# Performance work log

Measured on AMD Instinct MI355X. Metric: run time of the kernel, lower is better.

The kernel has to match this reference:

```python
import jax, jax.numpy as jnp
import numpy as np

INPUT_DIM = 1024
EMBED_DIM = 1024
NUM_HEADS = 16
HEAD_DIM = EMBED_DIM // NUM_HEADS


def setup_inputs() -> dict:
    key = jax.random.key(0)
    k_x, k_qkv, k_w, k_b = jax.random.split(key, 4)
    B, N = 2, 2048
    x = jax.random.normal(k_x, (B, N, INPUT_DIM), dtype=jnp.float32)
    # nn.Linear weights: stored [out, in]; scale like torch default init
    s1 = 1.0 / np.sqrt(INPUT_DIM)
    s2 = 1.0 / np.sqrt(EMBED_DIM)
    W_qkv = jax.random.uniform(k_qkv, (3 * EMBED_DIM, INPUT_DIM), jnp.float32, -s1, s1)
    W_out = jax.random.uniform(k_w, (EMBED_DIM, EMBED_DIM), jnp.float32, -s2, s2)
    b_out = jax.random.uniform(k_b, (EMBED_DIM,), jnp.float32, -s2, s2)
    return {"x": x, "W_qkv": W_qkv, "W_out": W_out, "b_out": b_out}


def reference(x, W_qkv, W_out, b_out):
    B, N, C = x.shape
    # qkv projection (no bias): [B, N, 3*embed]
    qkv = jnp.einsum('bnc,ec->bne', x, W_qkv)
    q = qkv[:, :, 0:EMBED_DIM].reshape(B, N, NUM_HEADS, HEAD_DIM)
    k = qkv[:, :, EMBED_DIM:2 * EMBED_DIM].reshape(B, N, NUM_HEADS, HEAD_DIM)
    v = qkv[:, :, 2 * EMBED_DIM:3 * EMBED_DIM].reshape(B, N, NUM_HEADS, HEAD_DIM)
    scores = jnp.einsum('bihd,bjhd->bhij', q, k) / jnp.sqrt(jnp.float32(HEAD_DIM))
    attn = jax.nn.softmax(scores, axis=-1)
    out = jnp.einsum('bhij,bjhd->bihd', attn, v).reshape(B, N, EMBED_DIM)
    return jnp.einsum('bne,oe->bno', out, W_out) + b_out
```

## Files before the change

kernel.cpp:

```cpp
#include <hip/hip_runtime.h>
#include <stdint.h>

typedef __attribute__((ext_vector_type(8))) short short8;
typedef __attribute__((ext_vector_type(4))) short bf16x4;
typedef __attribute__((ext_vector_type(4))) float f32x4;

#define MFMA32(a, b, c) __builtin_amdgcn_mfma_f32_16x16x32_bf16((a), (b), (c), 0, 0, 0)

__device__ __forceinline__ uint16_t f32_to_bf16(float f) {
  union { float f; uint32_t u; } v; v.f = f;
  uint32_t u = v.u;
  u += 0x7FFFu + ((u >> 16) & 1u);
  return (uint16_t)(u >> 16);
}
__device__ __forceinline__ uint16_t f32_to_bf16_fast(float f) {
  union { float f; uint32_t u; } v; v.f = f;
  return (uint16_t)((v.u + 0x8000u) >> 16);
}

__device__ __forceinline__ void load_lds16(const uint16_t* g, uint16_t* l) {
  __builtin_amdgcn_global_load_lds(
      (const __attribute__((address_space(1))) uint32_t*)g,
      (__attribute__((address_space(3))) uint32_t*)l, 16, 0, 0);
}

__global__ __launch_bounds__(256) void cvt3_kernel(
    const float* __restrict__ x, const float* __restrict__ w1,
    const float* __restrict__ w2, uint16_t* __restrict__ xb,
    uint16_t* __restrict__ w1b, uint16_t* __restrict__ w2b) {
  const int i = blockIdx.x * 256 + threadIdx.x;
  const float4* src;
  ushort4* dst;
  int off;
  if (i < 1048576) { src = (const float4*)x;  dst = (ushort4*)xb;  off = i; }
  else if (i < 1835008) { src = (const float4*)w1; dst = (ushort4*)w1b; off = i - 1048576; }
  else { src = (const float4*)w2; dst = (ushort4*)w2b; off = i - 1835008; }
  const float4 v = src[off];
  ushort4 o;
  o.x = f32_to_bf16(v.x);
  o.y = f32_to_bf16(v.y);
  o.z = f32_to_bf16(v.z);
  o.w = f32_to_bf16(v.w);
  dst[off] = o;
}

__global__ __launch_bounds__(256) void gemm_qkv_kernel(
    const uint16_t* __restrict__ A, const uint16_t* __restrict__ Bt,
    uint16_t* __restrict__ Qh, uint16_t* __restrict__ Kh, uint16_t* __restrict__ Vh) {
  __shared__ __align__(16) uint16_t As[128 * 64];
  __shared__ __align__(16) uint16_t Bs[128 * 64];
  const int tid = threadIdx.x;
  const int wave = tid >> 6;
  const int lane = tid & 63;
  const int quad = lane >> 4;
  const int l16 = lane & 15;
  const int row0 = blockIdx.x * 128;
  const int col0 = blockIdx.y * 128;
  const int wm = (wave >> 1) * 64;
  const int wn = (wave & 1) * 64;
  const int K = 1024;

  f32x4 acc[4][4];
#pragma unroll
  for (int a = 0; a < 4; ++a)
#pragma unroll
    for (int b = 0; b < 4; ++b) acc[a][b] = (f32x4){0.f, 0.f, 0.f, 0.f};

  const int swz8 = ((lane & 7) ^ ((lane >> 3) & 7)) * 8;
  const uint16_t* gA = A + (size_t)(row0 + wave * 32 + (lane >> 3)) * K + swz8;
  const uint16_t* gB = Bt + (size_t)(col0 + wave * 32 + (lane >> 3)) * K + swz8;

  for (int k0 = 0; k0 < K; k0 += 64) {
#pragma unroll
    for (int s = 0; s < 4; ++s) {
      load_lds16(gA + (size_t)s * 8 * K + k0, &As[(wave * 32 + s * 8) * 64]);
      load_lds16(gB + (size_t)s * 8 * K + k0, &Bs[(wave * 32 + s * 8) * 64]);
    }
    __syncthreads();
#pragma unroll
    for (int ks = 0; ks < 2; ++ks) {
      const int cswz = (((ks * 4 + quad) ^ (l16 & 7)) * 8);
      short8 af[4], bf[4];
#pragma unroll
      for (int mt = 0; mt < 4; ++mt)
        af[mt] = *(const short8*)&As[(wm + mt * 16 + l16) * 64 + cswz];
#pragma unroll
      for (int nt = 0; nt < 4; ++nt)
        bf[nt] = *(const short8*)&Bs[(wn + nt * 16 + l16) * 64 + cswz];
#pragma unroll
      for (int mt = 0; mt < 4; ++mt)
#pragma unroll
        for (int nt = 0; nt < 4; ++nt)
          acc[mt][nt] = MFMA32(af[mt], bf[nt], acc[mt][nt]);
    }
    __syncthreads();
  }

#pragma unroll
  for (int mt = 0; mt < 4; ++mt) {
#pragma unroll
    for (int nt = 0; nt < 4; ++nt) {
      const int col = col0 + wn + nt * 16 + l16;
      const int which = col >> 10;
      const int hc = (col & 1023) >> 6;
      const int d = col & 63;
#pragma unroll
      for (int r = 0; r < 4; ++r) {
        const int row = row0 + wm + mt * 16 + quad * 4 + r;
        const float val = acc[mt][nt][r];
        const int b = row >> 11;
        const int nn = row & 2047;
        const size_t hb = (size_t)(b * 16 + hc) * 131072;
        if (which == 0) {
          Qh[hb + (size_t)nn * 64 + d] = f32_to_bf16(val * 0.1803368801111244f);
        } else if (which == 1) {
          const uint16_t bv = f32_to_bf16(val);
          const int jt = nn >> 6, st = (nn >> 4) & 3, j16 = nn & 15;
          const int kc = d >> 5, qd = (d >> 3) & 3, e = d & 7;
          Kh[hb + jt * 4096 + st * 1024 + kc * 512 + (qd * 16 + j16) * 8 + e] = bv;
        } else {
          const uint16_t bv = f32_to_bf16(val);
          const int jt = nn >> 6, jp = nn & 63;
          const int st2 = jp >> 5, j32 = jp & 31;
          const int qv = (j32 >> 2) & 3, e = (j32 >> 4) * 4 + (j32 & 3);
          const int dt = d >> 4, d16 = d & 15;
          Vh[hb + jt * 4096 + (st2 * 4 + dt) * 512 + (qv * 16 + d16) * 8 + e] = bv;
        }
      }
    }
  }
}

__global__ __launch_bounds__(256) void gemm_out_kernel(
    const uint16_t* __restrict__ A, const uint16_t* __restrict__ Bt,
    float* __restrict__ Cf, const float* __restrict__ bias) {
  __shared__ __align__(16) uint16_t As[128 * 64];
  __shared__ __align__(16) uint16_t Bs[64 * 64];
  const int tid = threadIdx.x;
  const int wave = tid >> 6;
  const int lane = tid & 63;
  const int quad = lane >> 4;
  const int l16 = lane & 15;
  const int row0 = blockIdx.x * 128;
  const int col0 = blockIdx.y * 64;
  const int wm = (wave >> 1) * 64;
  const int wn = (wave & 1) * 32;
  const int K = 1024;
  const int N = 1024;

  f32x4 acc[4][2];
#pragma unroll
  for (int a = 0; a < 4; ++a)
#pragma unroll
    for (int b = 0; b < 2; ++b) acc[a][b] = (f32x4){0.f, 0.f, 0.f, 0.f};

  const int swz8 = ((lane & 7) ^ ((lane >> 3) & 7)) * 8;
  const uint16_t* gA = A + (size_t)(row0 + wave * 32 + (lane >> 3)) * K + swz8;
  const uint16_t* gB = Bt + (size_t)(col0 + wave * 16 + (lane >> 3)) * K + swz8;

  for (int k0 = 0; k0 < K; k0 += 64) {
#pragma unroll
    for (int s = 0; s < 4; ++s)
      load_lds16(gA + (size_t)s * 8 * K + k0, &As[(wave * 32 + s * 8) * 64]);
#pragma unroll
    for (int s = 0; s < 2; ++s)
      load_lds16(gB + (size_t)s * 8 * K + k0, &Bs[(wave * 16 + s * 8) * 64]);
    __syncthreads();
#pragma unroll
    for (int ks = 0; ks < 2; ++ks) {
      const int cswz = (((ks * 4 + quad) ^ (l16 & 7)) * 8);
      short8 af[4], bf[2];
#pragma unroll
      for (int mt = 0; mt < 4; ++mt)
        af[mt] = *(const short8*)&As[(wm + mt * 16 + l16) * 64 + cswz];
#pragma unroll
      for (int nt = 0; nt < 2; ++nt)
        bf[nt] = *(const short8*)&Bs[(wn + nt * 16 + l16) * 64 + cswz];
#pragma unroll
      for (int mt = 0; mt < 4; ++mt)
#pragma unroll
        for (int nt = 0; nt < 2; ++nt)
          acc[mt][nt] = MFMA32(af[mt], bf[nt], acc[mt][nt]);
    }
    __syncthreads();
  }

#pragma unroll
  for (int mt = 0; mt < 4; ++mt) {
#pragma unroll
    for (int nt = 0; nt < 2; ++nt) {
      const int col = col0 + wn + nt * 16 + l16;
#pragma unroll
      for (int r = 0; r < 4; ++r) {
        const int row = row0 + wm + mt * 16 + quad * 4 + r;
        Cf[(size_t)row * N + col] = acc[mt][nt][r] + bias[col];
      }
    }
  }
}

__global__ __launch_bounds__(256, 4) void attn_kernel(
    const uint16_t* __restrict__ Qh, const uint16_t* __restrict__ Kh,
    const uint16_t* __restrict__ Vh, uint16_t* __restrict__ out) {
  __shared__ __align__(16) uint16_t Ks[2][4096];
  __shared__ __align__(16) uint16_t Vs[2][4096];
  const int tid = threadIdx.x;
  const int wave = tid >> 6;
  const int lane = tid & 63;
  const int quad = lane >> 4;
  const int l16 = lane & 15;
  const int bx = blockIdx.x;
  const int xcd = bx & 7;
  const int g = bx >> 3;
  const int it = g & 31;
  const int h = ((g >> 5) & 1) * 8 + xcd;
  const int ib = g >> 6;
  const int i0 = it * 64 + wave * 16;
  const size_t hb = (size_t)(ib * 16 + h) * 131072;

  short8 qf[2];
#pragma unroll
  for (int kc = 0; kc < 2; ++kc)
    qf[kc] = *(const short8*)(Qh + hb + (size_t)(i0 + l16) * 64 + kc * 32 + quad * 8);

  f32x4 o[4], o4;
  o4 = (f32x4){0.f, 0.f, 0.f, 0.f};
#pragma unroll
  for (int t = 0; t < 4; ++t) o[t] = (f32x4){0.f, 0.f, 0.f, 0.f};

  const short8 ones8 = {(short)0x3F80, (short)0x3F80, (short)0x3F80, (short)0x3F80,
                        (short)0x3F80, (short)0x3F80, (short)0x3F80, (short)0x3F80};

  const uint16_t* gK = Kh + hb + wave * 1024 + lane * 8;
  const uint16_t* gV = Vh + hb + wave * 1024 + lane * 8;
  const int so = wave * 1024;

  load_lds16(gK, &Ks[0][so]);
  load_lds16(gK + 512, &Ks[0][so + 512]);
  load_lds16(gV, &Vs[0][so]);
  load_lds16(gV + 512, &Vs[0][so + 512]);
  __syncthreads();

#pragma unroll 2
  for (int t = 0; t < 32; ++t) {
    const int cur = t & 1;
    if (t < 31) {
      const size_t goff = (size_t)(t + 1) * 4096;
      load_lds16(gK + goff, &Ks[cur ^ 1][so]);
      load_lds16(gK + goff + 512, &Ks[cur ^ 1][so + 512]);
      load_lds16(gV + goff, &Vs[cur ^ 1][so]);
      load_lds16(gV + goff + 512, &Vs[cur ^ 1][so + 512]);
    }

    short8 kf[8];
#pragma unroll
    for (int i = 0; i < 8; ++i) kf[i] = *(const short8*)&Ks[cur][i * 512 + lane * 8];

    f32x4 s[4];
#pragma unroll
    for (int st = 0; st < 4; ++st) {
      f32x4 sc = (f32x4){0.f, 0.f, 0.f, 0.f};
      sc = MFMA32(kf[st * 2 + 0], qf[0], sc);
      sc = MFMA32(kf[st * 2 + 1], qf[1], sc);
      s[st] = sc;
    }

    short8 v8[8];
#pragma unroll
    for (int i = 0; i < 8; ++i) v8[i] = *(const short8*)&Vs[cur][i * 512 + lane * 8];

    short8 p8[2];
#pragma unroll
    for (int st2 = 0; st2 < 2; ++st2) {
      short8 p;
#pragma unroll
      for (int hh = 0; hh < 2; ++hh)
#pragma unroll
        for (int r = 0; r < 4; ++r)
          p[hh * 4 + r] =
              (short)f32_to_bf16_fast(__builtin_amdgcn_exp2f(s[st2 * 2 + hh][r]));
      p8[st2] = p;
    }

#pragma unroll
    for (int st2 = 0; st2 < 2; ++st2) {
      o4 = MFMA32(p8[st2], ones8, o4);
#pragma unroll
      for (int dt = 0; dt < 4; ++dt)
        o[dt] = MFMA32(p8[st2], v8[st2 * 4 + dt], o[dt]);
    }

    __syncthreads();
  }

#pragma unroll
  for (int r = 0; r < 4; ++r) {
    const float inv = 1.0f / o4[r];
    const int row = i0 + quad * 4 + r;
    const size_t obase = (size_t)(ib * 2048 + row) * 1024 + h * 64;
#pragma unroll
    for (int tt = 0; tt < 4; ++tt)
      out[obase + tt * 16 + l16] = f32_to_bf16(o[tt][r] * inv);
  }
}

extern "C" void kernel_launch(void* const* d_in, const int* in_sizes, int n_in,
                              void* d_out, int out_size, void* d_ws, size_t ws_size,
                              hipStream_t stream) {
  const float* x = (const float*)d_in[0];
  const float* Wqkv = (const float*)d_in[1];
  const float* Wout = (const float*)d_in[2];
  const float* bout = (const float*)d_in[3];

  uint16_t* xb = (uint16_t*)d_ws;
  uint16_t* wqkvb = xb + (size_t)4096 * 1024;
  uint16_t* woutb = wqkvb + (size_t)3072 * 1024;
  uint16_t* qh = woutb + (size_t)1024 * 1024;
  uint16_t* kh = qh + (size_t)32 * 131072;
  uint16_t* vh = kh + (size_t)32 * 131072;
  uint16_t* attnb = vh + (size_t)32 * 131072;

  cvt3_kernel<<<8192, 256, 0, stream>>>(x, Wqkv, Wout, xb, wqkvb, woutb);

  gemm_qkv_kernel<<<dim3(4096 / 128, 3072 / 128), 256, 0, stream>>>(
      xb, wqkvb, qh, kh, vh);

  attn_kernel<<<1024, 256, 0, stream>>>(qh, kh, vh, attnb);

  gemm_out_kernel<<<dim3(4096 / 128, 1024 / 64), 256, 0, stream>>>(
      attnb, woutb, (float*)d_out, bout);
}
```

Before: 182.9 us.

## Store Q/K row-major in GEMM output and read them strided in attention

The QKV GEMM epilogue now writes Q and K contiguously into a row-major [tokens, 3072] buffer instead of scattering them into head-blocked, fragment-swizzled layouts, which is meant to make those stores coalesced. The attention kernel reads Q and K directly from this buffer with a 3072-element row stride, and the softmax scale moves from the Q store to the exp2 argument. The trade-off is less contiguous K tile loads in attention (16-byte chunks from rows 6 KB apart) plus an extra multiply per score.

```diff
diff --git a/kernel.cpp b/kernel.cpp
--- a/kernel.cpp
+++ b/kernel.cpp
@@ -46,7 +46,7 @@
 
 __global__ __launch_bounds__(256) void gemm_qkv_kernel(
     const uint16_t* __restrict__ A, const uint16_t* __restrict__ Bt,
-    uint16_t* __restrict__ Qh, uint16_t* __restrict__ Kh, uint16_t* __restrict__ Vh) {
+    uint16_t* __restrict__ qkv, uint16_t* __restrict__ Vh) {
   __shared__ __align__(16) uint16_t As[128 * 64];
   __shared__ __align__(16) uint16_t Bs[128 * 64];
   const int tid = threadIdx.x;
@@ -102,23 +102,18 @@
     for (int nt = 0; nt < 4; ++nt) {
       const int col = col0 + wn + nt * 16 + l16;
       const int which = col >> 10;
-      const int hc = (col & 1023) >> 6;
-      const int d = col & 63;
 #pragma unroll
       for (int r = 0; r < 4; ++r) {
         const int row = row0 + wm + mt * 16 + quad * 4 + r;
         const float val = acc[mt][nt][r];
-        const int b = row >> 11;
-        const int nn = row & 2047;
-        const size_t hb = (size_t)(b * 16 + hc) * 131072;
-        if (which == 0) {
-          Qh[hb + (size_t)nn * 64 + d] = f32_to_bf16(val * 0.1803368801111244f);
-        } else if (which == 1) {
-          const uint16_t bv = f32_to_bf16(val);
-          const int jt = nn >> 6, st = (nn >> 4) & 3, j16 = nn & 15;
-          const int kc = d >> 5, qd = (d >> 3) & 3, e = d & 7;
-          Kh[hb + jt * 4096 + st * 1024 + kc * 512 + (qd * 16 + j16) * 8 + e] = bv;
+        if (which < 2) {
+          qkv[(size_t)row * 3072 + col] = f32_to_bf16(val);
         } else {
+          const int hc = (col & 1023) >> 6;
+          const int d = col & 63;
+          const int b = row >> 11;
+          const int nn = row & 2047;
+          const size_t hb = (size_t)(b * 16 + hc) * 131072;
           const uint16_t bv = f32_to_bf16(val);
           const int jt = nn >> 6, jp = nn & 63;
           const int st2 = jp >> 5, j32 = jp & 31;
@@ -200,8 +195,8 @@
 }
 
 __global__ __launch_bounds__(256, 4) void attn_kernel(
-    const uint16_t* __restrict__ Qh, const uint16_t* __restrict__ Kh,
-    const uint16_t* __restrict__ Vh, uint16_t* __restrict__ out) {
+    const uint16_t* __restrict__ qkv, const uint16_t* __restrict__ Vh,
+    uint16_t* __restrict__ out) {
   __shared__ __align__(16) uint16_t Ks[2][4096];
   __shared__ __align__(16) uint16_t Vs[2][4096];
   const int tid = threadIdx.x;
@@ -216,12 +211,13 @@
   const int h = ((g >> 5) & 1) * 8 + xcd;
   const int ib = g >> 6;
   const int i0 = it * 64 + wave * 16;
-  const size_t hb = (size_t)(ib * 16 + h) * 131072;
+  const float SC = 0.1803368801111244f;
 
   short8 qf[2];
 #pragma unroll
   for (int kc = 0; kc < 2; ++kc)
-    qf[kc] = *(const short8*)(Qh + hb + (size_t)(i0 + l16) * 64 + kc * 32 + quad * 8);
+    qf[kc] = *(const short8*)(qkv + (size_t)(ib * 2048 + i0 + l16) * 3072 +
+                              h * 64 + kc * 32 + quad * 8);
 
   f32x4 o[4], o4;
   o4 = (f32x4){0.f, 0.f, 0.f, 0.f};
@@ -231,12 +227,13 @@
   const short8 ones8 = {(short)0x3F80, (short)0x3F80, (short)0x3F80, (short)0x3F80,
                         (short)0x3F80, (short)0x3F80, (short)0x3F80, (short)0x3F80};
 
-  const uint16_t* gK = Kh + hb + wave * 1024 + lane * 8;
-  const uint16_t* gV = Vh + hb + wave * 1024 + lane * 8;
+  const uint16_t* gK = qkv + (size_t)(ib * 2048 + wave * 16 + l16) * 3072 +
+                       1024 + h * 64 + quad * 8;
+  const uint16_t* gV = Vh + (size_t)(ib * 16 + h) * 131072 + wave * 1024 + lane * 8;
   const int so = wave * 1024;
 
   load_lds16(gK, &Ks[0][so]);
-  load_lds16(gK + 512, &Ks[0][so + 512]);
+  load_lds16(gK + 32, &Ks[0][so + 512]);
   load_lds16(gV, &Vs[0][so]);
   load_lds16(gV + 512, &Vs[0][so + 512]);
   __syncthreads();
@@ -245,11 +242,12 @@
   for (int t = 0; t < 32; ++t) {
     const int cur = t & 1;
     if (t < 31) {
-      const size_t goff = (size_t)(t + 1) * 4096;
-      load_lds16(gK + goff, &Ks[cur ^ 1][so]);
-      load_lds16(gK + goff + 512, &Ks[cur ^ 1][so + 512]);
-      load_lds16(gV + goff, &Vs[cur ^ 1][so]);
-      load_lds16(gV + goff + 512, &Vs[cur ^ 1][so + 512]);
+      const size_t koff = (size_t)(t + 1) * (64 * 3072);
+      const size_t voff = (size_t)(t + 1) * 4096;
+      load_lds16(gK + koff, &Ks[cur ^ 1][so]);
+      load_lds16(gK + koff + 32, &Ks[cur ^ 1][so + 512]);
+      load_lds16(gV + voff, &Vs[cur ^ 1][so]);
+      load_lds16(gV + voff + 512, &Vs[cur ^ 1][so + 512]);
     }
 
     short8 kf[8];
@@ -277,8 +275,8 @@
       for (int hh = 0; hh < 2; ++hh)
 #pragma unroll
         for (int r = 0; r < 4; ++r)
-          p[hh * 4 + r] =
-              (short)f32_to_bf16_fast(__builtin_amdgcn_exp2f(s[st2 * 2 + hh][r]));
+          p[hh * 4 + r] = (short)f32_to_bf16_fast(
+              __builtin_amdgcn_exp2f(s[st2 * 2 + hh][r] * SC));
       p8[st2] = p;
     }
 
@@ -315,17 +313,16 @@
   uint16_t* xb = (uint16_t*)d_ws;
   uint16_t* wqkvb = xb + (size_t)4096 * 1024;
   uint16_t* woutb = wqkvb + (size_t)3072 * 1024;
-  uint16_t* qh = woutb + (size_t)1024 * 1024;
-  uint16_t* kh = qh + (size_t)32 * 131072;
-  uint16_t* vh = kh + (size_t)32 * 131072;
+  uint16_t* qkvb = woutb + (size_t)1024 * 1024;
+  uint16_t* vh = qkvb + (size_t)4096 * 3072;
   uint16_t* attnb = vh + (size_t)32 * 131072;
 
   cvt3_kernel<<<8192, 256, 0, stream>>>(x, Wqkv, Wout, xb, wqkvb, woutb);
 
   gemm_qkv_kernel<<<dim3(4096 / 128, 3072 / 128), 256, 0, stream>>>(
-      xb, wqkvb, qh, kh, vh);
-
-  attn_kernel<<<1024, 256, 0, stream>>>(qh, kh, vh, attnb);
+      xb, wqkvb, qkvb, vh);
+
+  attn_kernel<<<1024, 256, 0, stream>>>(qkvb, vh, attnb);
 
   gemm_out_kernel<<<dim3(4096 / 128, 1024 / 64), 256, 0, stream>>>(
       attnb, woutb, (float*)d_out, bout);
```

Result: slower. 188.1 us (+2.8%).
